# Optimization experiments

Hardware: AMD Instinct MI355X
Metric: run time of the kernel (lower is better)

## Reference

```python
import jax, jax.numpy as jnp
import numpy as np

IN_MODES = (4, 4, 6, 8)  # prod = 768 = d_model; same modes for input and output
D_MODEL = 768
N_HEADS = 12
D_HEAD = D_MODEL // N_HEADS
SCALE = 1.0 / np.sqrt(D_HEAD)
TT_RANKS = (1, 32, 64, 32, 1)


def tt_linear(x, c0, c1, c2, c3, b):
    # TT-factorized linear: cores c_k have shape (r_{k-1}, m_k, n_k, r_k)
    # with in/out modes IN_MODES. x: [B, S, 768]
    B, S, D = x.shape
    t = x.reshape(B * S, *IN_MODES)                     # n i j k l over in-modes
    t = jnp.einsum('nijkl,mir->njklmr', t, c0[0])       # contract n1, r0=1 squeezed
    t = jnp.einsum('njklmr,rpjs->nklmps', t, c1)        # contract n2 and rank r1
    t = jnp.einsum('nklmps,sqkt->nlmpqt', t, c2)        # contract n3 and rank r2
    t = jnp.einsum('nlmpqt,tul->nmpqu', t, c3[..., 0])  # contract n4 and rank r3, r4=1
    return t.reshape(B, S, D) + b                        # out-modes m,p,q,u -> 768


def _make_tt_params(key):
    ks = jax.random.split(key, 4)
    cores = []
    for i in range(4):
        shape = (TT_RANKS[i], IN_MODES[i], IN_MODES[i], TT_RANKS[i + 1])
        cores.append(jax.random.normal(ks[i], shape, jnp.float32) * 0.05)
    bias = jnp.zeros((D_MODEL,), jnp.float32)
    return cores, bias


def setup_inputs() -> dict:
    key = jax.random.key(0)
    kx, kq, kk, kv, ko = jax.random.split(key, 5)
    B, S = 2, 2048
    x = jax.random.normal(kx, (B, S, D_MODEL), jnp.float32)
    mask = jnp.tril(jnp.ones((S, S), dtype=bool))[None, None]  # causal [1,1,S,S]
    out = {'x': x, 'mask': mask}
    for name, k in (('q', kq), ('k', kk), ('v', kv), ('o', ko)):
        cores, bias = _make_tt_params(k)
        for i in range(4):
            out[f'{name}c{i}'] = cores[i]
        out[f'{name}b'] = bias
    return out


def reference(x, mask,
              qc0, qc1, qc2, qc3, qb,
              kc0, kc1, kc2, kc3, kb,
              vc0, vc1, vc2, vc3, vb,
              oc0, oc1, oc2, oc3, ob):
    B, S, _ = x.shape
    q = tt_linear(x, qc0, qc1, qc2, qc3, qb)
    k = tt_linear(x, kc0, kc1, kc2, kc3, kb)
    v = tt_linear(x, vc0, vc1, vc2, vc3, vb)
    # [B, S, H, Dh] -> [B, H, S, Dh]
    q = q.reshape(B, S, N_HEADS, D_HEAD).transpose(0, 2, 1, 3)
    k = k.reshape(B, S, N_HEADS, D_HEAD).transpose(0, 2, 1, 3)
    v = v.reshape(B, S, N_HEADS, D_HEAD).transpose(0, 2, 1, 3)
    scores = jnp.einsum('bhqd,bhkd->bhqk', q, k) * SCALE  # full O(S^2) scores
    scores = jnp.where(mask, scores, jnp.float32(-10000.0))  # masked_fill(mask==0,-1e4)
    attn = jax.nn.softmax(scores, axis=-1)  # dropout is identity at eval
    out = jnp.einsum('bhqk,bhkd->bhqd', attn, v)
    out = out.transpose(0, 2, 1, 3).reshape(B, S, D_MODEL)
    return tt_linear(out, oc0, oc1, oc2, oc3, ob)
```

## Files before the change

### kernel.cpp

```cpp
#include <hip/hip_runtime.h>
#include <cstddef>
#include <cstdint>

#define D_MODEL 768
#define N_HEADS 12
#define SEQ 2048
#define BATCH 2
#define NROWS (BATCH * SEQ)
#define W_ELEMS (D_MODEL * D_MODEL)
#define Y_ELEMS (NROWS * D_MODEL)

typedef __attribute__((ext_vector_type(8))) short bf16x8;
typedef __attribute__((ext_vector_type(4))) float f32x4;

struct TTPtrs {
    const float* c0[4];
    const float* c1[4];
    const float* c2[4];
    const float* c3[4];
};

__device__ __forceinline__ float bf2f(uint16_t u) {
    union { uint32_t u; float f; } c; c.u = ((uint32_t)u) << 16; return c.f;
}
__device__ __forceinline__ uint16_t f2bf(float f) {
    union { float f; uint32_t u; } c; c.f = f;
    uint32_t x = c.u + 0x7fffu + ((c.u >> 16) & 1u);
    return (uint16_t)(x >> 16);
}
__device__ __forceinline__ uint32_t cvtpk(float lo, float hi) {
    uint32_t r;
    asm("v_cvt_pk_bf16_f32 %0, %1, %2" : "=v"(r) : "v"(lo), "v"(hi));
    return r;
}
__device__ __forceinline__ void glds16(const void* g, void* l) {
    auto gp = reinterpret_cast<const __attribute__((address_space(1))) uint32_t*>(
        reinterpret_cast<uintptr_t>(g));
    auto lp = reinterpret_cast<__attribute__((address_space(3))) uint32_t*>(
        reinterpret_cast<uintptr_t>(l));
    __builtin_amdgcn_global_load_lds(gp, lp, 16, 0, 0);
}

__global__ __launch_bounds__(256) void pre_kernel(TTPtrs P, float* __restrict__ wsA,
                                                  const float* __restrict__ x,
                                                  uint16_t* __restrict__ xb) {
    const int bx = blockIdx.x;
    if (bx < 256) {
        const int mat = bx >> 6;
        const float* c0 = P.c0[mat];
        const float* c1 = P.c1[mat];
        float* A = wsA + mat * 16384;
        int idx = (bx & 63) * 256 + threadIdx.x;
        int s = idx & 63, pj = (idx >> 6) & 15, mi = idx >> 10;
        float acc = 0.f;
        #pragma unroll 8
        for (int r = 0; r < 32; r++)
            acc = fmaf(c0[mi * 32 + r], c1[(r * 16 + pj) * 64 + s], acc);
        A[idx] = acc;
    } else {
        int idx = ((bx - 256) * 256 + threadIdx.x) * 4;
        float4 v = *(const float4*)(x + idx);
        *(uint2*)(xb + idx) = make_uint2(cvtpk(v.x, v.y), cvtpk(v.z, v.w));
    }
}

__global__ __launch_bounds__(256) void tt_buildB(TTPtrs P, const float* __restrict__ wsA,
                                                 float* __restrict__ wsB) {
    const int mat = blockIdx.y;
    const float* c2 = P.c2[mat];
    const float* A = wsA + mat * 16384;
    float* B = wsB + (size_t)mat * 294912;
    int idx = blockIdx.x * 256 + threadIdx.x;
    int t = idx & 31;
    int rest = idx >> 5;
    int qk = rest % 36;
    int rest2 = rest / 36;
    int pj = rest2 & 15, mi = rest2 >> 4;
    const float* Arow = A + (mi * 16 + pj) * 64;
    float acc = 0.f;
    #pragma unroll 8
    for (int s = 0; s < 64; s++)
        acc = fmaf(Arow[s], c2[(s * 36 + qk) * 32 + t], acc);
    B[idx] = acc;
}

__global__ __launch_bounds__(256) void tt_buildC(TTPtrs P, const float* __restrict__ wsB,
                                                 uint16_t* __restrict__ Wbf) {
    const int mat = blockIdx.z;
    const float* c3 = P.c3[mat];
    const float* B = wsB + (size_t)mat * 294912;
    uint16_t* Wt = Wbf + (size_t)mat * W_ELEMS;
    int in = blockIdx.x * 256 + threadIdx.x;
    int out = blockIdx.y;
    int u = out & 7, q = (out >> 3) % 6, p = (out / 48) & 3, m = out / 192;
    int l = in & 7,  k = (in >> 3) % 6,  j = (in / 48) & 3,  i = in / 192;
    int mi = m * 4 + i, pj = p * 4 + j, qk = q * 6 + k;
    const float* Brow = B + ((size_t)(mi * 16 + pj) * 36 + qk) * 32;
    const float* c3row = c3 + u * 8 + l;
    float acc = 0.f;
    #pragma unroll 8
    for (int t = 0; t < 32; t++)
        acc = fmaf(Brow[t], c3row[t * 64], acc);
    Wt[(size_t)out * D_MODEL + in] = f2bf(acc);
}

template <int MODE>
__global__ __launch_bounds__(256) void gemm_mfma(const uint16_t* __restrict__ X,
                                                 const uint16_t* __restrict__ Wall,
                                                 const float* __restrict__ b0,
                                                 const float* __restrict__ b1,
                                                 const float* __restrict__ b2,
                                                 void* __restrict__ Yall,
                                                 uint16_t* __restrict__ Vt) {
    __shared__ uint16_t lds[2][8192];
    const int z = blockIdx.z;
    const uint16_t* W = Wall + (size_t)z * W_ELEMS;
    const float* bias = (z == 0) ? b0 : (z == 1 ? b1 : b2);
    const int m0 = blockIdx.x * 128, n0 = blockIdx.y * 128;
    const int tid = threadIdx.x, w = tid >> 6, l = tid & 63;
    const int wr = w >> 1, wc = w & 1;
    const int l15 = l & 15, lg = l >> 4;

    const int srow = w * 32 + (l >> 2);
    const int scol = ((l & 3) ^ ((l >> 2) & 3)) * 8;
    const uint16_t* Abase = X + (size_t)(m0 + srow) * D_MODEL + scol;
    const uint16_t* Bbase = W + (size_t)(n0 + srow) * D_MODEL + scol;

    f32x4 acc[4][4];
    #pragma unroll
    for (int mi = 0; mi < 4; ++mi)
        #pragma unroll
        for (int ni = 0; ni < 4; ++ni) acc[mi][ni] = (f32x4){0.f, 0.f, 0.f, 0.f};

    auto stage = [&](int buf, int kt) {
        const uint16_t* A0 = Abase + kt * 32;
        const uint16_t* B0 = Bbase + kt * 32;
        glds16(A0, &lds[buf][w * 1024]);
        glds16(A0 + 16 * D_MODEL, &lds[buf][w * 1024 + 512]);
        glds16(B0, &lds[buf][4096 + w * 1024]);
        glds16(B0 + 16 * D_MODEL, &lds[buf][4096 + w * 1024 + 512]);
    };

    stage(0, 0);
    __syncthreads();
    const int roff = ((lg ^ (l & 3)) << 3);
    for (int kt = 0; kt < 24; ++kt) {
        int cur = kt & 1;
        if (kt < 23) stage(cur ^ 1, kt + 1);
        const uint16_t* As = &lds[cur][0];
        const uint16_t* Bs = &lds[cur][4096];
        bf16x8 a[4], bb[4];
        #pragma unroll
        for (int mi = 0; mi < 4; ++mi)
            a[mi] = *(const bf16x8*)(As + (wr * 64 + mi * 16 + l15) * 32 + roff);
        #pragma unroll
        for (int ni = 0; ni < 4; ++ni)
            bb[ni] = *(const bf16x8*)(Bs + (wc * 64 + ni * 16 + l15) * 32 + roff);
        #pragma unroll
        for (int mi = 0; mi < 4; ++mi)
            #pragma unroll
            for (int ni = 0; ni < 4; ++ni)
                acc[mi][ni] = __builtin_amdgcn_mfma_f32_16x16x32_bf16(
                    a[mi], bb[ni], acc[mi][ni], 0, 0, 0);
        __syncthreads();
    }

    float bv[4];
    #pragma unroll
    for (int ni = 0; ni < 4; ++ni) bv[ni] = bias[n0 + wc * 64 + ni * 16 + l15];

    if (MODE == 1 && z == 2) {
        #pragma unroll
        for (int mi = 0; mi < 4; ++mi) {
            int row = m0 + wr * 64 + mi * 16 + lg * 4;
            int bb_ = row >> 11, s = row & 2047;
            #pragma unroll
            for (int ni = 0; ni < 4; ++ni) {
                int col = n0 + wc * 64 + ni * 16 + l15;
                float v0 = acc[mi][ni][0] + bv[ni], v1 = acc[mi][ni][1] + bv[ni];
                float v2 = acc[mi][ni][2] + bv[ni], v3 = acc[mi][ni][3] + bv[ni];
                *(uint2*)(Vt + ((size_t)(bb_ * 12 + (col >> 6)) * 64 + (col & 63)) * 2048 + s) =
                    make_uint2(cvtpk(v0, v1), cvtpk(v2, v3));
            }
        }
    } else {
        #pragma unroll
        for (int mi = 0; mi < 4; ++mi)
            #pragma unroll
            for (int ni = 0; ni < 4; ++ni)
                #pragma unroll
                for (int r = 0; r < 4; ++r) {
                    int row = m0 + wr * 64 + mi * 16 + lg * 4 + r;
                    int col = n0 + wc * 64 + ni * 16 + l15;
                    float v = acc[mi][ni][r] + bv[ni];
                    if (MODE == 1)
                        ((uint16_t*)Yall + (size_t)z * Y_ELEMS)[(size_t)row * D_MODEL + col] = f2bf(v);
                    else
                        ((float*)Yall)[(size_t)row * D_MODEL + col] = v;
                }
    }
}

__global__ __launch_bounds__(256) void attn_mfma(const uint16_t* __restrict__ Q,
                                                 const uint16_t* __restrict__ K,
                                                 const uint16_t* __restrict__ Vt,
                                                 uint16_t* __restrict__ O) {
    __shared__ uint16_t ks[2][4096];
    __shared__ uint16_t vs[2][4096];
    __shared__ uint16_t ps[4][1024];

    const int bx = blockIdx.x;
    const int qt = 31 - bx / 24;
    const int bh = bx % 24;
    const int b = bh / 12, h = bh % 12;
    const int tid = threadIdx.x, w = tid >> 6, l = tid & 63;
    const int l15 = l & 15, lg = l >> 4;
    const size_t headoff = (size_t)b * SEQ * D_MODEL + h * 64;
    const size_t vhead = ((size_t)(b * 12 + h)) << 17;
    const int sc8 = ((l & 7) ^ ((l >> 3) & 7)) * 8;
    const int srow = w * 16 + (l >> 3);

    bf16x8 qf[2];
    {
        const uint16_t* qp = Q + headoff + (size_t)(qt * 64 + w * 16 + l15) * D_MODEL + lg * 8;
        #pragma unroll
        for (int ds = 0; ds < 2; ++ds) {
            bf16x8 qv = *(const bf16x8*)(qp + ds * 32);
            #pragma unroll
            for (int j = 0; j < 8; ++j)
                qf[ds][j] = (short)f2bf(bf2f((uint16_t)qv[j]) * 0.125f);
        }
    }

    float m_ = -3e38f, l_ = 0.f;
    f32x4 oacc[4];
    #pragma unroll
    for (int ni = 0; ni < 4; ++ni) oacc[ni] = (f32x4){0.f, 0.f, 0.f, 0.f};
    const int qglob = qt * 64 + w * 16 + l15;

    auto stage = [&](int buf, int kt) {
        const uint16_t* ksrc = K + headoff + (size_t)(kt * 64 + srow) * D_MODEL + sc8;
        glds16(ksrc, &ks[buf][w * 1024]);
        glds16(ksrc + 8 * D_MODEL, &ks[buf][w * 1024 + 512]);
        const uint16_t* vsrc = Vt + vhead + (size_t)srow * SEQ + kt * 64 + sc8;
        glds16(vsrc, &vs[buf][w * 1024]);
        glds16(vsrc + 8 * SEQ, &vs[buf][w * 1024 + 512]);
    };

    stage(0, 0);
    for (int kt = 0; kt <= qt; ++kt) {
        const int cur = kt & 1;
        __syncthreads();
        if (kt < qt) stage(cur ^ 1, kt + 1);

        f32x4 sacc[4];
        #pragma unroll
        for (int ki = 0; ki < 4; ++ki) sacc[ki] = (f32x4){0.f, 0.f, 0.f, 0.f};
        #pragma unroll
        for (int ds = 0; ds < 2; ++ds)
            #pragma unroll
            for (int ki = 0; ki < 4; ++ki) {
                int byte = (ki * 16 + l15) * 128 + ((((ds << 2) + lg) ^ (l15 & 7)) << 4);
                bf16x8 ak = *(const bf16x8*)((const char*)&ks[cur][0] + byte);
                sacc[ki] = __builtin_amdgcn_mfma_f32_16x16x32_bf16(ak, qf[ds], sacc[ki], 0, 0, 0);
            }

        const bool diag = (kt == qt);
        float sv[16];
        float mx = -3e38f;
        #pragma unroll
        for (int ki = 0; ki < 4; ++ki)
            #pragma unroll
            for (int r = 0; r < 4; ++r) {
                float s = sacc[ki][r];
                if (diag) {
                    int key = kt * 64 + ki * 16 + lg * 4 + r;
                    if (key > qglob) s = -3e38f;
                }
                sv[ki * 4 + r] = s;
                mx = fmaxf(mx, s);
            }
        mx = fmaxf(mx, __shfl_xor(mx, 16));
        mx = fmaxf(mx, __shfl_xor(mx, 32));
        if (__any(mx > m_ + 8.f)) {
            float mnew = fmaxf(m_, mx);
            float alpha = __expf(m_ - mnew);
            l_ *= alpha;
            float a0 = __shfl(alpha, lg * 4 + 0), a1 = __shfl(alpha, lg * 4 + 1);
            float a2 = __shfl(alpha, lg * 4 + 2), a3 = __shfl(alpha, lg * 4 + 3);
            #pragma unroll
            for (int ni = 0; ni < 4; ++ni) {
                oacc[ni][0] *= a0; oacc[ni][1] *= a1;
                oacc[ni][2] *= a2; oacc[ni][3] *= a3;
            }
            m_ = mnew;
        }
        float sum = 0.f;
        uint32_t pk[8];
        #pragma unroll
        for (int i = 0; i < 16; i += 2) {
            float p0 = __expf(sv[i] - m_);
            float p1 = __expf(sv[i + 1] - m_);
            sum += p0 + p1;
            pk[i >> 1] = cvtpk(p0, p1);
        }
        sum += __shfl_xor(sum, 16);
        sum += __shfl_xor(sum, 32);
        l_ += sum;

        uint16_t* psw = &ps[w][0];
        #pragma unroll
        for (int ki = 0; ki < 4; ++ki) {
            int byte = (l15 * 128 + ki * 32 + lg * 8) ^ ((l15 & 7) << 4);
            *(uint2*)((char*)psw + byte) = make_uint2(pk[ki * 2], pk[ki * 2 + 1]);
        }
        asm volatile("s_waitcnt lgkmcnt(0)" ::: "memory");
        __builtin_amdgcn_sched_barrier(0);

        #pragma unroll
        for (int kss = 0; kss < 2; ++kss) {
            int pbyte = l15 * 128 + ((((kss << 2) + lg) ^ (l15 & 7)) << 4);
            bf16x8 ap = *(const bf16x8*)((const char*)psw + pbyte);
            #pragma unroll
            for (int ni = 0; ni < 4; ++ni) {
                int vbyte = (ni * 16 + l15) * 128 + ((((kss << 2) + lg) ^ (l15 & 7)) << 4);
                bf16x8 bv = *(const bf16x8*)((const char*)&vs[cur][0] + vbyte);
                oacc[ni] = __builtin_amdgcn_mfma_f32_16x16x32_bf16(ap, bv, oacc[ni], 0, 0, 0);
            }
        }
    }

    float li0 = 1.f / __shfl(l_, lg * 4 + 0), li1 = 1.f / __shfl(l_, lg * 4 + 1);
    float li2 = 1.f / __shfl(l_, lg * 4 + 2), li3 = 1.f / __shfl(l_, lg * 4 + 3);
    #pragma unroll
    for (int ni = 0; ni < 4; ++ni) {
        int col = h * 64 + ni * 16 + l15;
        size_t rb = (size_t)(b * SEQ + qt * 64 + w * 16 + lg * 4) * D_MODEL + col;
        O[rb + 0 * D_MODEL] = f2bf(oacc[ni][0] * li0);
        O[rb + 1 * D_MODEL] = f2bf(oacc[ni][1] * li1);
        O[rb + 2 * D_MODEL] = f2bf(oacc[ni][2] * li2);
        O[rb + 3 * D_MODEL] = f2bf(oacc[ni][3] * li3);
    }
}

extern "C" void kernel_launch(void* const* d_in, const int* in_sizes, int n_in,
                              void* d_out, int out_size, void* d_ws, size_t ws_size,
                              hipStream_t stream) {
    const float* x = (const float*)d_in[0];
    TTPtrs P;
    const float* biases[4];
    const int base[4] = {2, 7, 12, 17};
    for (int t = 0; t < 4; t++) {
        P.c0[t] = (const float*)d_in[base[t] + 0];
        P.c1[t] = (const float*)d_in[base[t] + 1];
        P.c2[t] = (const float*)d_in[base[t] + 2];
        P.c3[t] = (const float*)d_in[base[t] + 3];
        biases[t] = (const float*)d_in[base[t] + 4];
    }

    char* ws = (char*)d_ws;
    float* wsA = (float*)(ws + 0);
    float* wsB = (float*)(ws + 262144);
    uint16_t* Wbf = (uint16_t*)(ws + 4980736);
    uint16_t* xbf = (uint16_t*)(ws + 9699328);
    uint16_t* Qbf = (uint16_t*)(ws + 15990784);
    uint16_t* Kbf = (uint16_t*)(ws + 22282240);
    uint16_t* Vtbf = (uint16_t*)(ws + 28573696);
    uint16_t* Obf = (uint16_t*)(ws + 34865152);
    (void)Kbf;

    pre_kernel<<<dim3(256 + 3072), 256, 0, stream>>>(P, wsA, x, xbf);
    tt_buildB<<<dim3(1152, 4), 256, 0, stream>>>(P, wsA, wsB);
    tt_buildC<<<dim3(3, 768, 4), 256, 0, stream>>>(P, wsB, Wbf);

    gemm_mfma<1><<<dim3(32, 6, 3), 256, 0, stream>>>(xbf, Wbf, biases[0], biases[1],
                                                     biases[2], (void*)Qbf, Vtbf);
    attn_mfma<<<dim3(24 * 32), 256, 0, stream>>>(Qbf, Kbf, Vtbf, Obf);

    gemm_mfma<0><<<dim3(32, 6, 1), 256, 0, stream>>>(Obf, Wbf + 3 * (size_t)W_ELEMS,
                                                     biases[3], biases[3], biases[3],
                                                     d_out, nullptr);
}
```

Baseline: 243.4 us.

## Stage TT core slices in LDS for weight build; use exp2 softmax and MFMA priority

The final TT weight-construction kernel now assigns one block per (mi,pj) slice and stages that slice's B data and the c3 core in shared memory before computing a 48x48 output tile. This replaces scattered global reads per output element. The attention kernel folds log2(e) into the Q scale so it can use the hardware exp2 instruction, adjusting the rescale threshold to match. It also raises wave priority around the MFMA sections to favour matrix issue. The grid for the weight build drops from about 9k blocks to 1k blocks, which lowers parallelism in exchange for data reuse.

```diff
diff --git a/kernel.cpp b/kernel.cpp
--- a/kernel.cpp
+++ b/kernel.cpp
@@ -86,22 +86,40 @@
 
 __global__ __launch_bounds__(256) void tt_buildC(TTPtrs P, const float* __restrict__ wsB,
                                                  uint16_t* __restrict__ Wbf) {
-    const int mat = blockIdx.z;
+    __shared__ float b_lds[36 * 33];
+    __shared__ float c_lds[32 * 64];
+    const int mat = blockIdx.y;
+    const int mipj = blockIdx.x;
+    const int mi = mipj >> 4, pj = mipj & 15;
+    const int m = mi >> 2, i = mi & 3, p = pj >> 2, j = pj & 3;
+    const float* Bsrc = wsB + (size_t)mat * 294912 + (size_t)mipj * 1152;
     const float* c3 = P.c3[mat];
-    const float* B = wsB + (size_t)mat * 294912;
     uint16_t* Wt = Wbf + (size_t)mat * W_ELEMS;
-    int in = blockIdx.x * 256 + threadIdx.x;
-    int out = blockIdx.y;
-    int u = out & 7, q = (out >> 3) % 6, p = (out / 48) & 3, m = out / 192;
-    int l = in & 7,  k = (in >> 3) % 6,  j = (in / 48) & 3,  i = in / 192;
-    int mi = m * 4 + i, pj = p * 4 + j, qk = q * 6 + k;
-    const float* Brow = B + ((size_t)(mi * 16 + pj) * 36 + qk) * 32;
-    const float* c3row = c3 + u * 8 + l;
-    float acc = 0.f;
-    #pragma unroll 8
-    for (int t = 0; t < 32; t++)
-        acc = fmaf(Brow[t], c3row[t * 64], acc);
-    Wt[(size_t)out * D_MODEL + in] = f2bf(acc);
+    const int tid = threadIdx.x;
+
+    for (int e = tid; e < 1152; e += 256) {
+        int qk = e >> 5, t = e & 31;
+        b_lds[qk * 33 + t] = Bsrc[e];
+    }
+    for (int e = tid; e < 2048; e += 256)
+        c_lds[e] = c3[e];
+    __syncthreads();
+
+    const int outbase = (m * 4 + p) * 48;
+    const int inbase = (i * 4 + j) * 48;
+    #pragma unroll
+    for (int n = 0; n < 9; n++) {
+        int idx = n * 256 + tid;
+        int qu = idx / 48, kl = idx % 48;
+        int q = qu >> 3, u = qu & 7, k = kl >> 3, l = kl & 7;
+        const float* brow = &b_lds[(q * 6 + k) * 33];
+        const float* crow = &c_lds[u * 8 + l];
+        float acc = 0.f;
+        #pragma unroll 8
+        for (int t = 0; t < 32; t++)
+            acc = fmaf(brow[t], crow[t * 64], acc);
+        Wt[(size_t)(outbase + qu) * D_MODEL + inbase + kl] = f2bf(acc);
+    }
 }
 
 template <int MODE>
@@ -220,6 +238,7 @@
     const int sc8 = ((l & 7) ^ ((l >> 3) & 7)) * 8;
     const int srow = w * 16 + (l >> 3);
 
+    const float QS = 0.125f * 1.44269504088896f;
     bf16x8 qf[2];
     {
         const uint16_t* qp = Q + headoff + (size_t)(qt * 64 + w * 16 + l15) * D_MODEL + lg * 8;
@@ -228,7 +247,7 @@
             bf16x8 qv = *(const bf16x8*)(qp + ds * 32);
             #pragma unroll
             for (int j = 0; j < 8; ++j)
-                qf[ds][j] = (short)f2bf(bf2f((uint16_t)qv[j]) * 0.125f);
+                qf[ds][j] = (short)f2bf(bf2f((uint16_t)qv[j]) * QS);
         }
     }
 
@@ -256,6 +275,7 @@
         f32x4 sacc[4];
         #pragma unroll
         for (int ki = 0; ki < 4; ++ki) sacc[ki] = (f32x4){0.f, 0.f, 0.f, 0.f};
+        __builtin_amdgcn_s_setprio(1);
         #pragma unroll
         for (int ds = 0; ds < 2; ++ds)
             #pragma unroll
@@ -264,6 +284,7 @@
                 bf16x8 ak = *(const bf16x8*)((const char*)&ks[cur][0] + byte);
                 sacc[ki] = __builtin_amdgcn_mfma_f32_16x16x32_bf16(ak, qf[ds], sacc[ki], 0, 0, 0);
             }
+        __builtin_amdgcn_s_setprio(0);
 
         const bool diag = (kt == qt);
         float sv[16];
@@ -282,9 +303,9 @@
             }
         mx = fmaxf(mx, __shfl_xor(mx, 16));
         mx = fmaxf(mx, __shfl_xor(mx, 32));
-        if (__any(mx > m_ + 8.f)) {
+        if (__any(mx > m_ + 11.54f)) {
             float mnew = fmaxf(m_, mx);
-            float alpha = __expf(m_ - mnew);
+            float alpha = __builtin_amdgcn_exp2f(m_ - mnew);
             l_ *= alpha;
             float a0 = __shfl(alpha, lg * 4 + 0), a1 = __shfl(alpha, lg * 4 + 1);
             float a2 = __shfl(alpha, lg * 4 + 2), a3 = __shfl(alpha, lg * 4 + 3);
@@ -299,8 +320,8 @@
         uint32_t pk[8];
         #pragma unroll
         for (int i = 0; i < 16; i += 2) {
-            float p0 = __expf(sv[i] - m_);
-            float p1 = __expf(sv[i + 1] - m_);
+            float p0 = __builtin_amdgcn_exp2f(sv[i] - m_);
+            float p1 = __builtin_amdgcn_exp2f(sv[i + 1] - m_);
             sum += p0 + p1;
             pk[i >> 1] = cvtpk(p0, p1);
         }
@@ -317,6 +338,7 @@
         asm volatile("s_waitcnt lgkmcnt(0)" ::: "memory");
         __builtin_amdgcn_sched_barrier(0);
 
+        __builtin_amdgcn_s_setprio(1);
         #pragma unroll
         for (int kss = 0; kss < 2; ++kss) {
             int pbyte = l15 * 128 + ((((kss << 2) + lg) ^ (l15 & 7)) << 4);
@@ -328,6 +350,7 @@
                 oacc[ni] = __builtin_amdgcn_mfma_f32_16x16x32_bf16(ap, bv, oacc[ni], 0, 0, 0);
             }
         }
+        __builtin_amdgcn_s_setprio(0);
     }
 
     float li0 = 1.f / __shfl(l_, lg * 4 + 0), li1 = 1.f / __shfl(l_, lg * 4 + 1);
@@ -371,7 +394,7 @@
 
     pre_kernel<<<dim3(256 + 3072), 256, 0, stream>>>(P, wsA, x, xbf);
     tt_buildB<<<dim3(1152, 4), 256, 0, stream>>>(P, wsA, wsB);
-    tt_buildC<<<dim3(3, 768, 4), 256, 0, stream>>>(P, wsB, Wbf);
+    tt_buildC<<<dim3(256, 4), 256, 0, stream>>>(P, wsB, Wbf);
 
     gemm_mfma<1><<<dim3(32, 6, 3), 256, 0, stream>>>(xbf, Wbf, biases[0], biases[1],
                                                      biases[2], (void*)Qbf, Vtbf);
```

Measured after the change: 239.8 us. No clear change (-1.5%).
